# Kernel optimization log

Hardware: AMD Instinct MI355X
Metric: run time of the kernel (lower is better)

The kernel has to match this reference:

```python
import jax, jax.numpy as jnp
import numpy as np

N, E, IN_CH, EDGE_DIM, OUT_CH = 50000, 600000, 128, 64, 128


def setup_inputs() -> dict:
    key = jax.random.key(0)
    ks = jax.random.split(key, 9)
    return {
        "x": jax.random.normal(ks[0], (N, IN_CH), dtype=jnp.float32),
        "edge_index": jax.random.randint(ks[1], (2, E), 0, N, dtype=jnp.int64),
        "edge_attr": jax.random.normal(ks[2], (E, EDGE_DIM), dtype=jnp.float32),
        "Wx": jax.random.normal(ks[3], (IN_CH, OUT_CH), dtype=jnp.float32) * 0.05,
        "bx": jax.random.normal(ks[4], (OUT_CH,), dtype=jnp.float32) * 0.05,
        "We": jax.random.normal(ks[5], (EDGE_DIM, OUT_CH), dtype=jnp.float32) * 0.05,
        "be": jax.random.normal(ks[6], (OUT_CH,), dtype=jnp.float32) * 0.05,
        "Wm": jax.random.normal(ks[7], (2 * OUT_CH, OUT_CH), dtype=jnp.float32) * 0.05,
        "bm": jax.random.normal(ks[8], (OUT_CH,), dtype=jnp.float32) * 0.05,
        "beta": jnp.float32(0.1),
    }


def reference(x, edge_index, edge_attr, Wx, bx, We, be, Wm, bm, beta):
    # node / edge projections
    xp = x @ Wx + bx                      # [N, out]
    ef = edge_attr @ We + be              # [E, out]
    src, dst = edge_index[0], edge_index[1]
    # gather source node features, combine with edge features
    msg = jnp.concatenate([xp[src], ef], axis=1)   # [E, 2*out]
    msg = jax.nn.leaky_relu(msg @ Wm + bm)         # slope 0.01 matches torch default
    # scatter-add into destination nodes
    agg = jax.ops.segment_sum(msg, dst, num_segments=xp.shape[0])  # [N, out]
    return jax.nn.sigmoid(agg) * jax.nn.relu(beta)
```

## Files before the change

kernel.cpp:

```cpp
#include <hip/hip_runtime.h>


#define NB 3125
#define NB_SHIFT 4
#define TPW 4

typedef __bf16 bf16x8 __attribute__((ext_vector_type(8)));
typedef float  f32x4  __attribute__((ext_vector_type(4)));
typedef unsigned short ushort_t;
typedef unsigned int   uint_t;

__device__ __forceinline__ ushort_t f2b(float f) {
    uint_t u = __float_as_uint(f);
    u += 0x7FFF + ((u >> 16) & 1);
    return (ushort_t)(u >> 16);
}
__device__ __forceinline__ uint_t pack2(float a, float b) {
    return (uint_t)f2b(a) | ((uint_t)f2b(b) << 16);
}
__device__ __forceinline__ float b2f(ushort_t v) {
    return __uint_as_float((uint_t)v << 16);
}

__global__ void fuse_weights_kernel(const float* __restrict__ Wx,
                                    const float* __restrict__ bx,
                                    const float* __restrict__ We,
                                    const float* __restrict__ be,
                                    const float* __restrict__ Wm,
                                    const float* __restrict__ bm,
                                    ushort_t* __restrict__ WxmT16,
                                    ushort_t* __restrict__ WemT16,
                                    float* __restrict__ bf) {
    int idx = blockIdx.x * blockDim.x + threadIdx.x;
    if (idx < 128 * 128) {
        int r = idx >> 7, c = idx & 127;
        float acc = 0.f;
        #pragma unroll 8
        for (int j = 0; j < 128; ++j) acc += Wx[r * 128 + j] * Wm[j * 128 + c];
        WxmT16[c * 128 + r] = f2b(acc);
    } else if (idx < 128 * 128 + 64 * 128) {
        int t = idx - 128 * 128;
        int r = t >> 7, c = t & 127;
        float acc = 0.f;
        #pragma unroll 8
        for (int j = 0; j < 128; ++j) acc += We[r * 128 + j] * Wm[(128 + j) * 128 + c];
        WemT16[c * 64 + r] = f2b(acc);
    } else if (idx < 128 * 128 + 64 * 128 + 128) {
        int c = idx - (128 * 128 + 64 * 128);
        float acc = bm[c];
        #pragma unroll 8
        for (int j = 0; j < 128; ++j)
            acc += bx[j] * Wm[j * 128 + c] + be[j] * Wm[(128 + j) * 128 + c];
        bf[c] = acc;
    }
}

__global__ __launch_bounds__(256) void node_gemm_kernel(
        const float* __restrict__ x, const ushort_t* __restrict__ WxmT16,
        const float* __restrict__ bf, ushort_t* __restrict__ ub, int N) {
    int tid = threadIdx.x;
    int g = blockIdx.x * 4 + (tid >> 6);
    if (g >= (N / 16) * 2) return;
    int lane = tid & 63, l15 = lane & 15, quad = lane >> 4;
    int n0 = (g >> 1) * 16;
    int chBase = (g & 1) * 64;

    bf16x8 B[4][4];
    #pragma unroll
    for (int ct = 0; ct < 4; ++ct)
        #pragma unroll
        for (int kk = 0; kk < 4; ++kk)
            B[ct][kk] = __builtin_bit_cast(bf16x8, *((const uint4*)
                &WxmT16[(size_t)(chBase + ct * 16 + l15) * 128 + kk * 32 + quad * 8]));

    bf16x8 A[4];
    #pragma unroll
    for (int kk = 0; kk < 4; ++kk) {
        const float4* s = (const float4*)&x[(size_t)(n0 + l15) * 128 + kk * 32 + quad * 8];
        float4 v0 = s[0], v1 = s[1];
        uint4 w;
        w.x = pack2(v0.x, v0.y);
        w.y = pack2(v0.z, v0.w);
        w.z = pack2(v1.x, v1.y);
        w.w = pack2(v1.z, v1.w);
        A[kk] = __builtin_bit_cast(bf16x8, w);
    }

    f32x4 acc[4] = {{0.f,0.f,0.f,0.f},{0.f,0.f,0.f,0.f},
                    {0.f,0.f,0.f,0.f},{0.f,0.f,0.f,0.f}};
    #pragma unroll
    for (int kk = 0; kk < 4; ++kk)
        #pragma unroll
        for (int ct = 0; ct < 4; ++ct)
            acc[ct] = __builtin_amdgcn_mfma_f32_16x16x32_bf16(A[kk], B[ct][kk], acc[ct], 0, 0, 0);

    #pragma unroll
    for (int ct = 0; ct < 4; ++ct) {
        float bias = bf[chBase + ct * 16 + l15];
        #pragma unroll
        for (int r = 0; r < 4; ++r)
            ub[(size_t)(n0 + quad * 4 + r) * 128 + chBase + ct * 16 + l15] =
                f2b(acc[ct][r] + bias);
    }
}

__global__ __launch_bounds__(1024) void hist_kernel(
        const int* __restrict__ ei, int* __restrict__ cnt, int E) {
    __shared__ int lcnt[NB];
    int t = threadIdx.x;
    for (int i = t; i < NB; i += 1024) lcnt[i] = 0;
    __syncthreads();
    int base = blockIdx.x * 8192;
    #pragma unroll
    for (int j = 0; j < 8; ++j) {
        int e = base + t + j * 1024;
        if (e < E) atomicAdd(&lcnt[ei[E + e] >> NB_SHIFT], 1);
    }
    __syncthreads();
    for (int i = t; i < NB; i += 1024) {
        int c = lcnt[i];
        if (c) atomicAdd(&cnt[i], c);
    }
}

__global__ __launch_bounds__(1024) void scan_kernel(
        const int* __restrict__ cnt, int* __restrict__ start,
        int* __restrict__ cur, int nb, int E) {
    __shared__ int tot[1024];
    int t = threadIdx.x;
    int v[4]; int sum = 0;
    #pragma unroll
    for (int j = 0; j < 4; ++j) {
        int i = t * 4 + j;
        v[j] = (i < nb) ? cnt[i] : 0;
        sum += v[j];
    }
    tot[t] = sum;
    __syncthreads();
    for (int d = 1; d < 1024; d <<= 1) {
        int val = tot[t];
        int add = (t >= d) ? tot[t - d] : 0;
        __syncthreads();
        tot[t] = val + add;
        __syncthreads();
    }
    int ex = (t == 0) ? 0 : tot[t - 1];
    #pragma unroll
    for (int j = 0; j < 4; ++j) {
        int i = t * 4 + j;
        if (i < nb) { start[i] = ex; cur[i] = ex; }
        ex += v[j];
    }
    if (t == 1023) start[nb] = ex;
}

__global__ __launch_bounds__(1024) void binpos_kernel(
        const int* __restrict__ ei, int* __restrict__ cur,
        int* __restrict__ pos, uint_t* __restrict__ recs, int E) {
    __shared__ int lcnt[NB];
    __shared__ int lbase[NB];
    int t = threadIdx.x;
    for (int i = t; i < NB; i += 1024) lcnt[i] = 0;
    __syncthreads();
    int base = blockIdx.x * 8192;
    int myrank[8], mybkt[8];
    #pragma unroll
    for (int j = 0; j < 8; ++j) {
        int e = base + t + j * 1024;
        if (e < E) {
            int b = ei[E + e] >> NB_SHIFT;
            mybkt[j] = b;
            myrank[j] = atomicAdd(&lcnt[b], 1);
        }
    }
    __syncthreads();
    for (int i = t; i < NB; i += 1024) {
        int c = lcnt[i];
        lbase[i] = c ? atomicAdd(&cur[i], c) : 0;
    }
    __syncthreads();
    #pragma unroll
    for (int j = 0; j < 8; ++j) {
        int e = base + t + j * 1024;
        if (e < E) {
            int p = lbase[mybkt[j]] + myrank[j];
            pos[e] = p;
            uint_t src  = (uint_t)ei[e];
            uint_t dstl = (uint_t)(ei[E + e] & ((1 << NB_SHIFT) - 1));
            recs[p] = src | (dstl << 16);
        }
    }
}

__global__ void copy_ea_kernel(const float* __restrict__ ea,
                               const int* __restrict__ pos,
                               ushort_t* __restrict__ eabs, int E8) {
    int gid = blockIdx.x * blockDim.x + threadIdx.x;
    if (gid >= E8) return;
    int e = gid >> 3, seg = gid & 7;
    int p = pos[e];
    const float4* s = (const float4*)ea + (size_t)e * 16 + seg * 2;
    float4 v0 = s[0], v1 = s[1];
    uint4 w;
    w.x = pack2(v0.x, v0.y);
    w.y = pack2(v0.z, v0.w);
    w.z = pack2(v1.x, v1.y);
    w.w = pack2(v1.z, v1.w);
    *((uint4*)&eabs[(size_t)p * 64 + seg * 8]) = w;
}

__global__ __launch_bounds__(256) void msg_stream_kernel(
        const ushort_t* __restrict__ eabs, const ushort_t* __restrict__ WemT16,
        ushort_t* __restrict__ msgl, int E) {
    int tid = threadIdx.x;
    int g = blockIdx.x * 4 + (tid >> 6);
    int grp = g >> 1;
    int chBase = (g & 1) << 6;
    int t0 = grp * (TPW * 16);
    if (t0 >= E) return;
    int lane = tid & 63, l15 = lane & 15, quad = lane >> 4;

    bf16x8 B[4][2];
    #pragma unroll
    for (int ct = 0; ct < 4; ++ct)
        #pragma unroll
        for (int kk = 0; kk < 2; ++kk)
            B[ct][kk] = __builtin_bit_cast(bf16x8, *((const uint4*)
                &WemT16[(size_t)(chBase + ct * 16 + l15) * 64 + kk * 32 + quad * 8]));

    #pragma unroll
    for (int tt = 0; tt < TPW; ++tt) {
        int t16 = t0 + tt * 16;
        if (t16 >= E) break;
        bf16x8 a0 = __builtin_bit_cast(bf16x8,
            *((const uint4*)&eabs[(size_t)(t16 + l15) * 64 + quad * 8]));
        bf16x8 a1 = __builtin_bit_cast(bf16x8,
            *((const uint4*)&eabs[(size_t)(t16 + l15) * 64 + 32 + quad * 8]));

        f32x4 acc[4] = {{0.f,0.f,0.f,0.f},{0.f,0.f,0.f,0.f},
                        {0.f,0.f,0.f,0.f},{0.f,0.f,0.f,0.f}};
        #pragma unroll
        for (int ct = 0; ct < 4; ++ct)
            acc[ct] = __builtin_amdgcn_mfma_f32_16x16x32_bf16(a0, B[ct][0], acc[ct], 0, 0, 0);
        #pragma unroll
        for (int ct = 0; ct < 4; ++ct)
            acc[ct] = __builtin_amdgcn_mfma_f32_16x16x32_bf16(a1, B[ct][1], acc[ct], 0, 0, 0);

        #pragma unroll
        for (int r = 0; r < 4; ++r) {
            int row = t16 + quad * 4 + r;
            #pragma unroll
            for (int ct = 0; ct < 4; ++ct)
                msgl[(size_t)row * 128 + chBase + ct * 16 + l15] = f2b(acc[ct][r]);
        }
    }
}

__global__ __launch_bounds__(512) void segsum_kernel(
        const ushort_t* __restrict__ msgl, const ushort_t* __restrict__ ub,
        const uint_t* __restrict__ recs, const int* __restrict__ start,
        const float* __restrict__ beta, float* __restrict__ out, int N) {
    __shared__ float accum[4][16][128];
    int tid = threadIdx.x;
    int b = blockIdx.x;
    int base = b << NB_SHIFT;

    for (int li = tid; li < 4 * 16 * 128; li += 512) ((float*)accum)[li] = 0.f;
    __syncthreads();

    int q = tid >> 7, ch = tid & 127;
    int s0 = start[b], s1 = start[b + 1];

    int p = s0 + q;
    uint_t rec = (p < s1) ? recs[p] : 0u;
    while (p < s1) {
        int pn = p + 4;
        uint_t recn = (pn < s1) ? recs[pn] : 0u;
        int sr = (int)(rec & 0xFFFF);
        int dl = (int)(rec >> 16);
        float mv  = b2f(msgl[(size_t)p * 128 + ch]);
        float uvv = b2f(ub[(size_t)sr * 128 + ch]);
        float m = mv + uvv;
        m = m > 0.f ? m : 0.01f * m;
        accum[q][dl][ch] += m;
        p = pn; rec = recn;
    }
    __syncthreads();

    float rb = beta[0];
    rb = rb > 0.f ? rb : 0.f;
    int r = tid >> 5, c4 = tid & 31;
    int n = base + r;
    if (n < N) {
        float4 v0 = *((float4*)&accum[0][r][c4 * 4]);
        float4 v1 = *((float4*)&accum[1][r][c4 * 4]);
        float4 v2 = *((float4*)&accum[2][r][c4 * 4]);
        float4 v3 = *((float4*)&accum[3][r][c4 * 4]);
        float4 v;
        v.x = v0.x + v1.x + v2.x + v3.x;
        v.y = v0.y + v1.y + v2.y + v3.y;
        v.z = v0.z + v1.z + v2.z + v3.z;
        v.w = v0.w + v1.w + v2.w + v3.w;
        v.x = rb / (1.f + __expf(-v.x));
        v.y = rb / (1.f + __expf(-v.y));
        v.z = rb / (1.f + __expf(-v.z));
        v.w = rb / (1.f + __expf(-v.w));
        ((float4*)out)[(size_t)n * 32 + c4] = v;
    }
}

extern "C" void kernel_launch(void* const* d_in, const int* in_sizes, int n_in,
                              void* d_out, int out_size, void* d_ws, size_t ws_size,
                              hipStream_t stream) {
    const float* x    = (const float*)d_in[0];
    const int*   ei   = (const int*)d_in[1];
    const float* ea   = (const float*)d_in[2];
    const float* Wx   = (const float*)d_in[3];
    const float* bx   = (const float*)d_in[4];
    const float* We   = (const float*)d_in[5];
    const float* be   = (const float*)d_in[6];
    const float* Wm   = (const float*)d_in[7];
    const float* bm   = (const float*)d_in[8];
    const float* beta = (const float*)d_in[9];

    int N = in_sizes[0] / 128;
    int E = in_sizes[2] / 64;

    float* out = (float*)d_out;

    char* ws = (char*)d_ws;
    ushort_t* WxmT16 = (ushort_t*)(ws);
    ushort_t* WemT16 = (ushort_t*)(ws + 32768);
    float*    bf     = (float*)(ws + 49152);
    ushort_t* ub     = (ushort_t*)(ws + 65536);
    size_t off = 65536 + (size_t)N * 128 * 2;
    ushort_t* eabs = (ushort_t*)(ws + off);
    off += (size_t)E * 64 * 2;
    uint_t* recs   = (uint_t*)(ws + off);
    off += (size_t)E * 4;
    int* pos       = (int*)(ws + off);
    off += (size_t)E * 4;
    int* cnt       = (int*)(ws + off);
    int* startb    = (int*)(ws + off + 16384);
    int* cur       = (int*)(ws + off + 32768);
    ushort_t* msgl = (ushort_t*)(ws + off + 49152);

    hipMemsetAsync(cnt, 0, (size_t)NB * sizeof(int), stream);

    fuse_weights_kernel<<<(24704 + 255) / 256, 256, 0, stream>>>(
        Wx, bx, We, be, Wm, bm, WxmT16, WemT16, bf);

    node_gemm_kernel<<<(N / 16 * 2 + 3) / 4, 256, 0, stream>>>(
        x, WxmT16, bf, ub, N);

    int nbBlocks = (E + 8191) / 8192;
    hist_kernel<<<nbBlocks, 1024, 0, stream>>>(ei, cnt, E);
    scan_kernel<<<1, 1024, 0, stream>>>(cnt, startb, cur, NB, E);
    binpos_kernel<<<nbBlocks, 1024, 0, stream>>>(ei, cur, pos, recs, E);

    int E8 = E * 8;
    copy_ea_kernel<<<(E8 + 255) / 256, 256, 0, stream>>>(ea, pos, eabs, E8);

    int ntile  = (E + 15) / 16;
    int ngrp   = (ntile + TPW - 1) / TPW;
    int nwaves = ngrp * 2;
    msg_stream_kernel<<<(nwaves + 3) / 4, 256, 0, stream>>>(
        eabs, WemT16, msgl, E);

    segsum_kernel<<<NB, 512, 0, stream>>>(
        msgl, ub, recs, startb, beta, out, N);
}
```

Baseline: 526.3 us.

## Fuse edge-attr conversion into message GEMM and use wave-per-bucket segment sum

Removes the separate copy kernel that permuted and converted edge attributes to bf16. The message GEMM now reads fp32 edge_attr directly in original order, converts it in registers, and scatters its bf16 output rows to their sorted positions via pos. Buckets shrink from 16 nodes to 2 nodes, so one wave handles a bucket, accumulates in registers with masked weights, and reduces across lane halves with a shuffle, dropping the shared-memory accumulator. The trade-off is scattered output writes in the GEMM, a larger histogram and scan (25 elements per thread), and a 25000-int shared array in binpos that reuses lcnt for the base offsets.

```diff
diff --git a/kernel.cpp b/kernel.cpp
--- a/kernel.cpp
+++ b/kernel.cpp
@@ -1,8 +1,8 @@
 #include <hip/hip_runtime.h>
 
 
-#define NB 3125
-#define NB_SHIFT 4
+#define NB 25000
+#define NB_SHIFT 1
 #define TPW 4
 
 typedef __bf16 bf16x8 __attribute__((ext_vector_type(8)));
@@ -17,9 +17,6 @@
 }
 __device__ __forceinline__ uint_t pack2(float a, float b) {
     return (uint_t)f2b(a) | ((uint_t)f2b(b) << 16);
-}
-__device__ __forceinline__ float b2f(ushort_t v) {
-    return __uint_as_float((uint_t)v << 16);
 }
 
 __global__ void fuse_weights_kernel(const float* __restrict__ Wx,
@@ -128,10 +125,10 @@
         int* __restrict__ cur, int nb, int E) {
     __shared__ int tot[1024];
     int t = threadIdx.x;
-    int v[4]; int sum = 0;
-    #pragma unroll
-    for (int j = 0; j < 4; ++j) {
-        int i = t * 4 + j;
+    int v[25]; int sum = 0;
+    #pragma unroll
+    for (int j = 0; j < 25; ++j) {
+        int i = t * 25 + j;
         v[j] = (i < nb) ? cnt[i] : 0;
         sum += v[j];
     }
@@ -146,8 +143,8 @@
     }
     int ex = (t == 0) ? 0 : tot[t - 1];
     #pragma unroll
-    for (int j = 0; j < 4; ++j) {
-        int i = t * 4 + j;
+    for (int j = 0; j < 25; ++j) {
+        int i = t * 25 + j;
         if (i < nb) { start[i] = ex; cur[i] = ex; }
         ex += v[j];
     }
@@ -158,7 +155,6 @@
         const int* __restrict__ ei, int* __restrict__ cur,
         int* __restrict__ pos, uint_t* __restrict__ recs, int E) {
     __shared__ int lcnt[NB];
-    __shared__ int lbase[NB];
     int t = threadIdx.x;
     for (int i = t; i < NB; i += 1024) lcnt[i] = 0;
     __syncthreads();
@@ -176,14 +172,14 @@
     __syncthreads();
     for (int i = t; i < NB; i += 1024) {
         int c = lcnt[i];
-        lbase[i] = c ? atomicAdd(&cur[i], c) : 0;
+        lcnt[i] = c ? atomicAdd(&cur[i], c) : 0;
     }
     __syncthreads();
     #pragma unroll
     for (int j = 0; j < 8; ++j) {
         int e = base + t + j * 1024;
         if (e < E) {
-            int p = lbase[mybkt[j]] + myrank[j];
+            int p = lcnt[mybkt[j]] + myrank[j];
             pos[e] = p;
             uint_t src  = (uint_t)ei[e];
             uint_t dstl = (uint_t)(ei[E + e] & ((1 << NB_SHIFT) - 1));
@@ -192,26 +188,9 @@
     }
 }
 
-__global__ void copy_ea_kernel(const float* __restrict__ ea,
-                               const int* __restrict__ pos,
-                               ushort_t* __restrict__ eabs, int E8) {
-    int gid = blockIdx.x * blockDim.x + threadIdx.x;
-    if (gid >= E8) return;
-    int e = gid >> 3, seg = gid & 7;
-    int p = pos[e];
-    const float4* s = (const float4*)ea + (size_t)e * 16 + seg * 2;
-    float4 v0 = s[0], v1 = s[1];
-    uint4 w;
-    w.x = pack2(v0.x, v0.y);
-    w.y = pack2(v0.z, v0.w);
-    w.z = pack2(v1.x, v1.y);
-    w.w = pack2(v1.z, v1.w);
-    *((uint4*)&eabs[(size_t)p * 64 + seg * 8]) = w;
-}
-
 __global__ __launch_bounds__(256) void msg_stream_kernel(
-        const ushort_t* __restrict__ eabs, const ushort_t* __restrict__ WemT16,
-        ushort_t* __restrict__ msgl, int E) {
+        const float* __restrict__ ea, const int* __restrict__ pos,
+        const ushort_t* __restrict__ WemT16, ushort_t* __restrict__ msgl, int E) {
     int tid = threadIdx.x;
     int g = blockIdx.x * 4 + (tid >> 6);
     int grp = g >> 1;
@@ -232,10 +211,23 @@
     for (int tt = 0; tt < TPW; ++tt) {
         int t16 = t0 + tt * 16;
         if (t16 >= E) break;
-        bf16x8 a0 = __builtin_bit_cast(bf16x8,
-            *((const uint4*)&eabs[(size_t)(t16 + l15) * 64 + quad * 8]));
-        bf16x8 a1 = __builtin_bit_cast(bf16x8,
-            *((const uint4*)&eabs[(size_t)(t16 + l15) * 64 + 32 + quad * 8]));
+        const float* rowp = &ea[(size_t)(t16 + l15) * 64];
+        const float4* sA = (const float4*)(rowp + quad * 8);
+        float4 v0 = sA[0], v1 = sA[1];
+        uint4 w0;
+        w0.x = pack2(v0.x, v0.y);
+        w0.y = pack2(v0.z, v0.w);
+        w0.z = pack2(v1.x, v1.y);
+        w0.w = pack2(v1.z, v1.w);
+        bf16x8 a0 = __builtin_bit_cast(bf16x8, w0);
+        const float4* sB = (const float4*)(rowp + 32 + quad * 8);
+        float4 v2 = sB[0], v3 = sB[1];
+        uint4 w1;
+        w1.x = pack2(v2.x, v2.y);
+        w1.y = pack2(v2.z, v2.w);
+        w1.z = pack2(v3.x, v3.y);
+        w1.w = pack2(v3.z, v3.w);
+        bf16x8 a1 = __builtin_bit_cast(bf16x8, w1);
 
         f32x4 acc[4] = {{0.f,0.f,0.f,0.f},{0.f,0.f,0.f,0.f},
                         {0.f,0.f,0.f,0.f},{0.f,0.f,0.f,0.f}};
@@ -246,66 +238,82 @@
         for (int ct = 0; ct < 4; ++ct)
             acc[ct] = __builtin_amdgcn_mfma_f32_16x16x32_bf16(a1, B[ct][1], acc[ct], 0, 0, 0);
 
+        int4 pr = *(const int4*)&pos[t16 + quad * 4];
+        int prr[4] = {pr.x, pr.y, pr.z, pr.w};
         #pragma unroll
         for (int r = 0; r < 4; ++r) {
-            int row = t16 + quad * 4 + r;
             #pragma unroll
             for (int ct = 0; ct < 4; ++ct)
-                msgl[(size_t)row * 128 + chBase + ct * 16 + l15] = f2b(acc[ct][r]);
+                msgl[(size_t)prr[r] * 128 + chBase + ct * 16 + l15] = f2b(acc[ct][r]);
         }
     }
 }
 
-__global__ __launch_bounds__(512) void segsum_kernel(
+__global__ __launch_bounds__(256) void segsum_kernel(
         const ushort_t* __restrict__ msgl, const ushort_t* __restrict__ ub,
         const uint_t* __restrict__ recs, const int* __restrict__ start,
         const float* __restrict__ beta, float* __restrict__ out, int N) {
-    __shared__ float accum[4][16][128];
-    int tid = threadIdx.x;
-    int b = blockIdx.x;
-    int base = b << NB_SHIFT;
-
-    for (int li = tid; li < 4 * 16 * 128; li += 512) ((float*)accum)[li] = 0.f;
-    __syncthreads();
-
-    int q = tid >> 7, ch = tid & 127;
-    int s0 = start[b], s1 = start[b + 1];
-
-    int p = s0 + q;
+    int wid = blockIdx.x * 4 + (threadIdx.x >> 6);
+    if (wid >= NB) return;
+    int lane = threadIdx.x & 63;
+    int half = lane >> 5;
+    int c8 = lane & 31;
+
+    int s0 = start[wid], s1 = start[wid + 1];
+    float a0[4] = {0.f, 0.f, 0.f, 0.f};
+    float a1[4] = {0.f, 0.f, 0.f, 0.f};
+
+    int p = s0 + half;
     uint_t rec = (p < s1) ? recs[p] : 0u;
     while (p < s1) {
-        int pn = p + 4;
+        int pn = p + 2;
         uint_t recn = (pn < s1) ? recs[pn] : 0u;
-        int sr = (int)(rec & 0xFFFF);
-        int dl = (int)(rec >> 16);
-        float mv  = b2f(msgl[(size_t)p * 128 + ch]);
-        float uvv = b2f(ub[(size_t)sr * 128 + ch]);
-        float m = mv + uvv;
-        m = m > 0.f ? m : 0.01f * m;
-        accum[q][dl][ch] += m;
+
+        uint2 mv = *(const uint2*)&msgl[(size_t)p * 128 + (c8 << 2)];
+        int sr = (int)(rec & 0xFFFFu);
+        uint2 uv = *(const uint2*)&ub[(size_t)sr * 128 + (c8 << 2)];
+
+        float w1 = (rec >> 16) ? 1.f : 0.f;
+        float w0 = 1.f - w1;
+
+        float m0 = __uint_as_float(mv.x << 16)         + __uint_as_float(uv.x << 16);
+        float m1 = __uint_as_float(mv.x & 0xFFFF0000u) + __uint_as_float(uv.x & 0xFFFF0000u);
+        float m2 = __uint_as_float(mv.y << 16)         + __uint_as_float(uv.y << 16);
+        float m3 = __uint_as_float(mv.y & 0xFFFF0000u) + __uint_as_float(uv.y & 0xFFFF0000u);
+        m0 = fmaxf(m0, 0.01f * m0);
+        m1 = fmaxf(m1, 0.01f * m1);
+        m2 = fmaxf(m2, 0.01f * m2);
+        m3 = fmaxf(m3, 0.01f * m3);
+
+        a0[0] += m0 * w0;  a1[0] += m0 * w1;
+        a0[1] += m1 * w0;  a1[1] += m1 * w1;
+        a0[2] += m2 * w0;  a1[2] += m2 * w1;
+        a0[3] += m3 * w0;  a1[3] += m3 * w1;
+
         p = pn; rec = recn;
     }
-    __syncthreads();
+
+    #pragma unroll
+    for (int j = 0; j < 4; ++j) {
+        a0[j] += __shfl_xor(a0[j], 32);
+        a1[j] += __shfl_xor(a1[j], 32);
+    }
 
     float rb = beta[0];
     rb = rb > 0.f ? rb : 0.f;
-    int r = tid >> 5, c4 = tid & 31;
-    int n = base + r;
+    int n = (wid << 1) + half;
     if (n < N) {
-        float4 v0 = *((float4*)&accum[0][r][c4 * 4]);
-        float4 v1 = *((float4*)&accum[1][r][c4 * 4]);
-        float4 v2 = *((float4*)&accum[2][r][c4 * 4]);
-        float4 v3 = *((float4*)&accum[3][r][c4 * 4]);
         float4 v;
-        v.x = v0.x + v1.x + v2.x + v3.x;
-        v.y = v0.y + v1.y + v2.y + v3.y;
-        v.z = v0.z + v1.z + v2.z + v3.z;
-        v.w = v0.w + v1.w + v2.w + v3.w;
+        if (half == 0) {
+            v.x = a0[0]; v.y = a0[1]; v.z = a0[2]; v.w = a0[3];
+        } else {
+            v.x = a1[0]; v.y = a1[1]; v.z = a1[2]; v.w = a1[3];
+        }
         v.x = rb / (1.f + __expf(-v.x));
         v.y = rb / (1.f + __expf(-v.y));
         v.z = rb / (1.f + __expf(-v.z));
         v.w = rb / (1.f + __expf(-v.w));
-        ((float4*)out)[(size_t)n * 32 + c4] = v;
+        ((float4*)out)[(size_t)n * 32 + c8] = v;
     }
 }
 
@@ -334,16 +342,14 @@
     float*    bf     = (float*)(ws + 49152);
     ushort_t* ub     = (ushort_t*)(ws + 65536);
     size_t off = 65536 + (size_t)N * 128 * 2;
-    ushort_t* eabs = (ushort_t*)(ws + off);
-    off += (size_t)E * 64 * 2;
     uint_t* recs   = (uint_t*)(ws + off);
     off += (size_t)E * 4;
     int* pos       = (int*)(ws + off);
     off += (size_t)E * 4;
     int* cnt       = (int*)(ws + off);
-    int* startb    = (int*)(ws + off + 16384);
-    int* cur       = (int*)(ws + off + 32768);
-    ushort_t* msgl = (ushort_t*)(ws + off + 49152);
+    int* startb    = (int*)(ws + off + 131072);
+    int* cur       = (int*)(ws + off + 262144);
+    ushort_t* msgl = (ushort_t*)(ws + off + 393216);
 
     hipMemsetAsync(cnt, 0, (size_t)NB * sizeof(int), stream);
 
@@ -358,15 +364,12 @@
     scan_kernel<<<1, 1024, 0, stream>>>(cnt, startb, cur, NB, E);
     binpos_kernel<<<nbBlocks, 1024, 0, stream>>>(ei, cur, pos, recs, E);
 
-    int E8 = E * 8;
-    copy_ea_kernel<<<(E8 + 255) / 256, 256, 0, stream>>>(ea, pos, eabs, E8);
-
     int ntile  = (E + 15) / 16;
     int ngrp   = (ntile + TPW - 1) / TPW;
     int nwaves = ngrp * 2;
     msg_stream_kernel<<<(nwaves + 3) / 4, 256, 0, stream>>>(
-        eabs, WemT16, msgl, E);
-
-    segsum_kernel<<<NB, 512, 0, stream>>>(
+        ea, pos, WemT16, msgl, E);
+
+    segsum_kernel<<<(NB + 3) / 4, 256, 0, stream>>>(
         msgl, ub, recs, startb, beta, out, N);
 }
```

Measured after the change: 481.0 us. 8.6% less time.
